# Kernel optimization log

Measured on AMD Instinct MI355X. Metric: run time of the kernel, lower is better.

Reference implementation:

```python
import math
import jax, jax.numpy as jnp
import numpy as np

B, N, D, H, PREFIX = 2, 2048, 2048, 16, 512
HD = D // H
ROPE_BASE = 10000.0

def _rope(x):
    # x: [b, h, n, d]; rotate-half RoPE with positions 0..n-1
    d = x.shape[-1]
    n = x.shape[-2]
    inv_freq = 1.0 / (ROPE_BASE ** (jnp.arange(0, d, 2, dtype=jnp.float32) / d))  # [d/2]
    pos = jnp.arange(n, dtype=jnp.float32)
    freqs = pos[:, None] * inv_freq[None, :]            # [n, d/2]
    cos, sin = jnp.cos(freqs), jnp.sin(freqs)
    x1, x2 = x[..., : d // 2], x[..., d // 2 :]
    return jnp.concatenate([x1 * cos - x2 * sin, x2 * cos + x1 * sin], axis=-1).astype(x.dtype)

def setup_inputs() -> dict:
    key = jax.random.key(0)
    ks = jax.random.split(key, 6)
    x = jax.random.normal(ks[0], (B, N, D), dtype=jnp.float32)
    prefix_k = jax.random.normal(ks[1], (B, H, PREFIX, HD), dtype=jnp.float32)
    prefix_v = jax.random.normal(ks[2], (B, H, PREFIX, HD), dtype=jnp.float32)
    Wqkv = jax.random.normal(ks[3], (D, 3 * D), dtype=jnp.float32) * (D ** -0.5)
    bqkv = jnp.zeros((3 * D,), dtype=jnp.float32)
    Wff = jax.random.normal(ks[4], (D, D), dtype=jnp.float32) * (D ** -0.5)
    bff = jnp.zeros((D,), dtype=jnp.float32)
    # causal mask over current tokens; prefix (cache) columns fully visible
    causal = jnp.tril(jnp.ones((N, N), dtype=jnp.int32))
    mask = jnp.concatenate([jnp.ones((N, PREFIX), dtype=jnp.int32), causal], axis=1)[None, None]  # [1,1,N,N+PREFIX]
    return {"x": x, "mask": mask, "prefix_k": prefix_k, "prefix_v": prefix_v,
            "Wqkv": Wqkv, "bqkv": bqkv, "Wff": Wff, "bff": bff}

def reference(x, mask, prefix_k, prefix_v, Wqkv, bqkv, Wff, bff):
    b, n, d = x.shape
    h = prefix_k.shape[1]
    hd = d // h
    qkv = (x @ Wqkv + bqkv).reshape(b, n, 3, h, hd)      # 'b n (c h d)'
    qkv = jnp.transpose(qkv, (2, 0, 3, 1, 4))            # -> c b h n d
    q, k, v = qkv[0], qkv[1], qkv[2]
    k = jnp.concatenate([prefix_k, k], axis=2)           # [b,h,kt,hd]
    v = jnp.concatenate([prefix_v, v], axis=2)
    next_prefix_kv = jnp.stack([k, v])                   # cached BEFORE rope (as in source)
    q = _rope(q)
    k = _rope(k)
    scores = jnp.einsum('bhqd,bhkd->bhqk', q, k) / math.sqrt(hd)
    scores = jnp.where(mask == 0, jnp.finfo(scores.dtype).min, scores)
    probs = jax.nn.softmax(scores, axis=-1)              # dropout_prob=0.0 -> identity
    attn_o = jnp.einsum('bhqk,bhkd->bhqd', probs, v)
    attn_o = jnp.transpose(attn_o, (0, 2, 1, 3)).reshape(b, n, d)
    return attn_o @ Wff + bff, next_prefix_kv
```

## Files before the change

kernel.cpp:

```cpp
#include <hip/hip_runtime.h>
#include <hip/hip_bf16.h>
#include <stdint.h>

#define TPB 256

using f32x4 = __attribute__((ext_vector_type(4))) float;
using s16x8 = __attribute__((ext_vector_type(8))) short;
using s16x4 = __attribute__((ext_vector_type(4))) short;

__device__ __forceinline__ short f2bf(float f){
  union { float f; uint32_t u; } v; v.f = f;
  uint32_t u = v.u;
  uint32_t r = (u + 0x7fffu + ((u >> 16) & 1u)) >> 16;
  return (short)(uint16_t)r;
}
__device__ __forceinline__ float bf2f(short b){
  union { uint32_t u; float f; } v; v.u = ((uint32_t)(uint16_t)b) << 16;
  return v.f;
}
__device__ __forceinline__ f32x4 mfma16(s16x8 a, s16x8 b, f32x4 c){
  return __builtin_amdgcn_mfma_f32_16x16x32_bf16(a, b, c, 0, 0, 0);
}

#define AS1(p) ((const __attribute__((address_space(1))) void*)(p))
#define AS3(p) ((__attribute__((address_space(3))) void*)(p))

__global__ void k_cvt_bf16(const float* __restrict__ src, short* __restrict__ dst, int n8){
  int i = blockIdx.x * TPB + threadIdx.x;
  if (i >= n8) return;
  const float4* s4 = (const float4*)src;
  float4 a = s4[2*i], b = s4[2*i+1];
  s16x8 o;
  o[0]=f2bf(a.x); o[1]=f2bf(a.y); o[2]=f2bf(a.z); o[3]=f2bf(a.w);
  o[4]=f2bf(b.x); o[5]=f2bf(b.y); o[6]=f2bf(b.z); o[7]=f2bf(b.w);
  *(s16x8*)(dst + 8*(size_t)i) = o;
}

__global__ void k_trans_cvt(const float* __restrict__ W, short* __restrict__ WT, int K, int Nn){
  __shared__ float ls[32][33];
  int k0 = blockIdx.x * 32, n0 = blockIdx.y * 32;
  int c = threadIdx.x & 31, i = threadIdx.x >> 5;
#pragma unroll
  for (int rr = 0; rr < 4; rr++){
    int row = i*4 + rr;
    ls[row][c] = W[(size_t)(k0+row)*Nn + n0 + c];
  }
  __syncthreads();
#pragma unroll
  for (int rr = 0; rr < 4; rr++){
    int ro = i*4 + rr;
    WT[(size_t)(n0+ro)*K + k0 + c] = f2bf(ls[c][ro]);
  }
}

template<int EPI>
__global__ void __launch_bounds__(512, 2) k_gemm8(
    const short* __restrict__ A, const short* __restrict__ Bt,
    int Nn, int K,
    const float* __restrict__ bias,
    float* __restrict__ outp,
    float* __restrict__ kvout,
    short* __restrict__ qpre, short* __restrict__ kpre, short* __restrict__ vpre)
{
  __shared__ __align__(16) short As[3][16384];
  __shared__ __align__(16) short Bs[3][8192];
  const int tid = threadIdx.x;
  const int w = tid >> 6, l = tid & 63;
  const int lrow = l & 15, lg = l >> 4;
  const int wm = w >> 1, wn = w & 1;
  const int m0 = blockIdx.x << 8, n0 = blockIdx.y << 7;
  const int NT = K >> 6;

  f32x4 acc[4][4] = {};

#define STAGE_A(slot, t, j) do {                                             \
    int chunk = ((w*4 + (j)) << 6) + l;                                      \
    int row = chunk >> 3, cc = chunk & 7;                                    \
    __builtin_amdgcn_global_load_lds(                                        \
      AS1(A + (size_t)(m0+row)*K + (t)*64 + ((cc ^ (row&7)) << 3)),          \
      AS3(&As[slot][(w*4 + (j)) << 9]), 16, 0, 0);                           \
  } while(0)
#define STAGE_B(slot, t, j) do {                                             \
    int chunk = ((w*2 + (j)) << 6) + l;                                      \
    int row = chunk >> 3, cc = chunk & 7;                                    \
    __builtin_amdgcn_global_load_lds(                                        \
      AS1(Bt + (size_t)(n0+row)*K + (t)*64 + ((cc ^ (row&7)) << 3)),         \
      AS3(&Bs[slot][(w*2 + (j)) << 9]), 16, 0, 0);                           \
  } while(0)

  STAGE_A(0,0,0); STAGE_A(0,0,1); STAGE_A(0,0,2); STAGE_A(0,0,3);
  STAGE_B(0,0,0); STAGE_B(0,0,1);
  STAGE_A(1,1,0); STAGE_A(1,1,1); STAGE_A(1,1,2); STAGE_A(1,1,3);
  STAGE_B(1,1,0); STAGE_B(1,1,1);

  int slot = 0;
  for (int t = 0; t < NT; ++t){
    if (t < NT-1) asm volatile("s_waitcnt vmcnt(6)" ::: "memory");
    else          asm volatile("s_waitcnt vmcnt(0)" ::: "memory");
    __builtin_amdgcn_s_barrier();
    asm volatile("" ::: "memory");
    const int sslot = (slot == 0) ? 2 : slot - 1;
    const bool st = (t+2) < NT;
    const char* ab = (const char*)As[slot];
    const char* bb = (const char*)Bs[slot];

    s16x8 bfr[4][2];
#pragma unroll
    for (int ni = 0; ni < 4; ni++){
      int row = wn*64 + ni*16 + lrow;
#pragma unroll
      for (int ks = 0; ks < 2; ks++)
        bfr[ni][ks] = *(const s16x8*)(bb + row*128 + ((ks*64 + lg*16) ^ ((row&7)<<4)));
    }
    s16x8 af[2][2];
#pragma unroll
    for (int mi = 0; mi < 2; mi++){
      int row = wm*64 + mi*16 + lrow;
#pragma unroll
      for (int ks = 0; ks < 2; ks++)
        af[mi][ks] = *(const s16x8*)(ab + row*128 + ((ks*64 + lg*16) ^ ((row&7)<<4)));
    }
    if (st){ STAGE_A(sslot,t+2,0); STAGE_A(sslot,t+2,1); STAGE_B(sslot,t+2,0); }
    __builtin_amdgcn_s_setprio(1);
#pragma unroll
    for (int ks = 0; ks < 2; ks++)
#pragma unroll
      for (int mi = 0; mi < 2; mi++)
#pragma unroll
        for (int ni = 0; ni < 4; ni++)
          acc[mi][ni] = mfma16(af[mi][ks], bfr[ni][ks], acc[mi][ni]);
    __builtin_amdgcn_s_setprio(0);
    asm volatile("" ::: "memory");
    __builtin_amdgcn_s_barrier();
    asm volatile("" ::: "memory");

    s16x8 af2[2][2];
#pragma unroll
    for (int mi = 0; mi < 2; mi++){
      int row = wm*64 + (mi+2)*16 + lrow;
#pragma unroll
      for (int ks = 0; ks < 2; ks++)
        af2[mi][ks] = *(const s16x8*)(ab + row*128 + ((ks*64 + lg*16) ^ ((row&7)<<4)));
    }
    if (st){ STAGE_A(sslot,t+2,2); STAGE_A(sslot,t+2,3); STAGE_B(sslot,t+2,1); }
    __builtin_amdgcn_s_setprio(1);
#pragma unroll
    for (int ks = 0; ks < 2; ks++)
#pragma unroll
      for (int mi = 0; mi < 2; mi++)
#pragma unroll
        for (int ni = 0; ni < 4; ni++)
          acc[mi+2][ni] = mfma16(af2[mi][ks], bfr[ni][ks], acc[mi+2][ni]);
    __builtin_amdgcn_s_setprio(0);
    slot = (slot == 2) ? 0 : slot + 1;
  }
#undef STAGE_A
#undef STAGE_B

#pragma unroll
  for (int mi = 0; mi < 4; mi++){
#pragma unroll
    for (int ni = 0; ni < 4; ni++){
      const int c  = n0 + wn*64 + ni*16 + lrow;
      const int mb = m0 + wm*64 + mi*16 + lg*4;
      const float bv = bias[c];
      if (EPI == 1){
#pragma unroll
        for (int r = 0; r < 4; r++)
          outp[(size_t)(mb+r)*Nn + c] = acc[mi][ni][r] + bv;
      } else {
        const int s = c >> 11, h = (c >> 7) & 15, tt = c & 127;
#pragma unroll
        for (int r = 0; r < 4; r++){
          const int m = mb + r;
          const int b = m >> 11, n = m & 2047;
          const int bh = b*16 + h;
          const float val = acc[mi][ni][r] + bv;
          if (s == 0){
            qpre[((size_t)bh*2048 + n)*128 + tt] = f2bf(val);
          } else if (s == 1){
            kvout[((size_t)bh*2560 + 512 + n)*128 + tt] = val;
            kpre[((size_t)bh*2048 + n)*128 + tt] = f2bf(val);
          } else {
            kvout[(size_t)(32 + bh)*327680 + (size_t)(512 + n)*128 + tt] = val;
            vpre[((size_t)bh*2048 + n)*128 + tt] = f2bf(val);
          }
        }
      }
    }
  }
}

__global__ void k_rope_k_new(const short* __restrict__ kpre, short* __restrict__ kr){
  int gid = blockIdx.x * TPB + threadIdx.x;
  int jb = (gid & 7) * 8; size_t row = gid >> 3;
  int bh = (int)(row >> 11), n = (int)(row & 2047);
  int pos = 512 + n;
  s16x8 v1 = *(const s16x8*)&kpre[row*128 + jb];
  s16x8 v2 = *(const s16x8*)&kpre[row*128 + 64 + jb];
  s16x8 o1, o2;
#pragma unroll
  for (int e = 0; e < 8; e++){
    float invf = __expf((float)(jb + e) * (-9.210340371976184f/64.0f));
    float sn, cs; __sincosf((float)pos * invf, &sn, &cs);
    float x1 = bf2f(v1[e]), x2 = bf2f(v2[e]);
    o1[e] = f2bf(x1*cs - x2*sn);
    o2[e] = f2bf(x2*cs + x1*sn);
  }
  size_t drow = (size_t)bh*2560 + pos;
  *(s16x8*)&kr[drow*128 + jb]      = o1;
  *(s16x8*)&kr[drow*128 + 64 + jb] = o2;
}

__global__ void k_rope_k_prefix(const float* __restrict__ pk, float* __restrict__ kvout0,
                                short* __restrict__ kr){
  int gid = blockIdx.x * TPB + threadIdx.x;
  int jb = (gid & 7) * 8; size_t row = gid >> 3;
  int bh = (int)(row >> 9), p = (int)(row & 511);
  float4 a1 = *(const float4*)&pk[row*128 + jb];
  float4 a2 = *(const float4*)&pk[row*128 + jb + 4];
  float4 b1 = *(const float4*)&pk[row*128 + 64 + jb];
  float4 b2 = *(const float4*)&pk[row*128 + 64 + jb + 4];
  size_t orow = (size_t)bh*2560 + p;
  *(float4*)&kvout0[orow*128 + jb]          = a1;
  *(float4*)&kvout0[orow*128 + jb + 4]      = a2;
  *(float4*)&kvout0[orow*128 + 64 + jb]     = b1;
  *(float4*)&kvout0[orow*128 + 64 + jb + 4] = b2;
  float x1[8] = {a1.x,a1.y,a1.z,a1.w,a2.x,a2.y,a2.z,a2.w};
  float x2[8] = {b1.x,b1.y,b1.z,b1.w,b2.x,b2.y,b2.z,b2.w};
  s16x8 o1, o2;
#pragma unroll
  for (int e = 0; e < 8; e++){
    float invf = __expf((float)(jb + e) * (-9.210340371976184f/64.0f));
    float sn, cs; __sincosf((float)p * invf, &sn, &cs);
    o1[e] = f2bf(x1[e]*cs - x2[e]*sn);
    o2[e] = f2bf(x2[e]*cs + x1[e]*sn);
  }
  *(s16x8*)&kr[orow*128 + jb]      = o1;
  *(s16x8*)&kr[orow*128 + 64 + jb] = o2;
}

__global__ void k_v_prefix(const float* __restrict__ pv, float* __restrict__ kvout1,
                           short* __restrict__ vT){
  __shared__ float ls[32][129];
  int bh = blockIdx.x >> 4, pt = blockIdx.x & 15;
  int p0 = pt*32, tid = threadIdx.x;
#pragma unroll
  for (int i = 0; i < 16; i++){
    int idx = i*TPB + tid; int p = idx >> 7, t = idx & 127;
    float v = pv[((size_t)bh*512 + p0 + p)*128 + t];
    ls[p][t] = v;
    kvout1[((size_t)bh*2560 + p0 + p)*128 + t] = v;
  }
  __syncthreads();
#pragma unroll
  for (int i = 0; i < 16; i++){
    int idx = i*TPB + tid; int t = idx >> 5, p = idx & 31;
    vT[((size_t)bh*128 + t)*2560 + p0 + p] = f2bf(ls[p][t]);
  }
}

__global__ void k_v_new(const short* __restrict__ vpre, short* __restrict__ vT){
  __shared__ float ls[32][129];
  int bh = blockIdx.x >> 6, nt = blockIdx.x & 63;
  int n0 = nt*32, tid = threadIdx.x;
#pragma unroll
  for (int i = 0; i < 16; i++){
    int idx = i*TPB + tid; int p = idx >> 7, t = idx & 127;
    ls[p][t] = bf2f(vpre[((size_t)bh*2048 + n0 + p)*128 + t]);
  }
  __syncthreads();
#pragma unroll
  for (int i = 0; i < 16; i++){
    int idx = i*TPB + tid; int t = idx >> 5, p = idx & 31;
    vT[((size_t)bh*128 + t)*2560 + 512 + n0 + p] = f2bf(ls[p][t]);
  }
}

__global__ void __launch_bounds__(256, 2) k_attn(
    const short* __restrict__ qr, const short* __restrict__ kr,
    const short* __restrict__ vT, short* __restrict__ attno)
{
  __shared__ short Ks[2][64*128];
  __shared__ short VTs[2][128*64];
  __shared__ short Ps[4][16*64];
  const int bh = blockIdx.x;
  const int pA = blockIdx.y, pB = 31 - pA;
  const int nA = 9 + pA, nTot = 49;
  const int tid = threadIdx.x, w = tid >> 6, l = tid & 63;
  const int lrow = l & 15, lg = l >> 4;
  const int b = bh >> 4, h = bh & 15;

  s16x8 qfA[4], qfB[4];
  {
    const int nAr = pA*64 + w*16 + lrow;
    const int nBr = pB*64 + w*16 + lrow;
    const size_t rA = (size_t)bh*2048 + nAr;
    const size_t rB = (size_t)bh*2048 + nBr;
#pragma unroll
    for (int ks = 0; ks < 4; ks++){
      qfA[ks] = *(const s16x8*)&qr[rA*128 + ks*32 + lg*8];
      qfB[ks] = *(const s16x8*)&qr[rB*128 + ks*32 + lg*8];
    }
    const float sc = 0.088388347648318447f;
#pragma unroll
    for (int ks = 0; ks < 2; ks++){
#pragma unroll
      for (int e = 0; e < 8; e++){
        const int j = ks*32 + lg*8 + e;
        const float invf = __expf((float)j * (-9.210340371976184f/64.0f));
        float sn, cs;
        __sincosf((float)nAr * invf, &sn, &cs);
        float x1 = bf2f(qfA[ks][e]), x2 = bf2f(qfA[ks+2][e]);
        qfA[ks][e]   = f2bf((x1*cs - x2*sn) * sc);
        qfA[ks+2][e] = f2bf((x2*cs + x1*sn) * sc);
        __sincosf((float)nBr * invf, &sn, &cs);
        float y1 = bf2f(qfB[ks][e]), y2 = bf2f(qfB[ks+2][e]);
        qfB[ks][e]   = f2bf((y1*cs - y2*sn) * sc);
        qfB[ks+2][e] = f2bf((y2*cs + y1*sn) * sc);
      }
    }
  }

#define STAGE_KV(buf, kv0s) do {                                                    \
    _Pragma("unroll")                                                               \
    for (int i_ = 0; i_ < 4; i_++){                                                 \
      int chunk = i_*256 + tid;                                                     \
      int row = chunk >> 4, cc = (chunk & 15) ^ (row & 7);                          \
      __builtin_amdgcn_global_load_lds(                                             \
        AS1(kr + ((size_t)bh*2560 + (kv0s) + row)*128 + cc*8),                      \
        AS3((char*)Ks[buf] + (i_*256 + w*64)*16), 16, 0, 0);                        \
    }                                                                               \
    _Pragma("unroll")                                                               \
    for (int i_ = 0; i_ < 4; i_++){                                                 \
      int chunk = i_*256 + tid;                                                     \
      int row = chunk >> 3, cc = (chunk & 7) ^ (row & 7);                           \
      __builtin_amdgcn_global_load_lds(                                             \
        AS1(vT + ((size_t)bh*128 + row)*2560 + (kv0s) + cc*8),                      \
        AS3((char*)VTs[buf] + (i_*256 + w*64)*16), 16, 0, 0);                       \
    }                                                                               \
  } while(0)

  STAGE_KV(0, 0);
  STAGE_KV(1, 64);

  char* psw = (char*)&Ps[w][0];
  int g = 0;
#pragma unroll 2
  for (int ph = 0; ph < 2; ph++){
    const int qt = ph ? pB : pA;
    const int n = 9 + qt;
    const int qbw = qt*64 + w*16;
    f32x4 acc[8] = {};
    float mr = -1e30f, lsum = 0.f;

    for (int t = 0; t < n; t++, g++){
      if (g+1 < nTot) asm volatile("s_waitcnt vmcnt(8)" ::: "memory");
      else            asm volatile("s_waitcnt vmcnt(0)" ::: "memory");
      __builtin_amdgcn_s_barrier();
      asm volatile("" ::: "memory");
      const char* kb_ = (const char*)Ks[g&1];
      const char* vb_ = (const char*)VTs[g&1];
      const int kv0 = t*64;

      f32x4 sf[4];
      __builtin_amdgcn_s_setprio(1);
#pragma unroll
      for (int kb = 0; kb < 4; kb++){
        f32x4 s = {0.f,0.f,0.f,0.f};
#pragma unroll
        for (int ks = 0; ks < 4; ks++){
          int row  = kb*16 + lrow;
          int colb = ks*64 + lg*16;
          s16x8 kf = *(const s16x8*)(kb_ + row*256 + (colb ^ ((row&7)<<4)));
          s = mfma16(kf, ph ? qfB[ks] : qfA[ks], s);
        }
        sf[kb] = s;
      }
      __builtin_amdgcn_s_setprio(0);

      const int qme = 512 + qbw + lrow;
      if (kv0 + 63 > 512 + qbw){
#pragma unroll
        for (int kb = 0; kb < 4; kb++)
#pragma unroll
          for (int r = 0; r < 4; r++){
            int kg = kv0 + kb*16 + lg*4 + r;
            if (kg > qme) sf[kb][r] = -1e30f;
          }
      }

      float m_ = fmaxf(
          fmaxf(fmaxf(fmaxf(sf[0][0],sf[0][1]),fmaxf(sf[0][2],sf[0][3])),
                fmaxf(fmaxf(sf[1][0],sf[1][1]),fmaxf(sf[1][2],sf[1][3]))),
          fmaxf(fmaxf(fmaxf(sf[2][0],sf[2][1]),fmaxf(sf[2][2],sf[2][3])),
                fmaxf(fmaxf(sf[3][0],sf[3][1]),fmaxf(sf[3][2],sf[3][3]))));
      m_ = fmaxf(m_, __shfl_xor(m_, 16));
      m_ = fmaxf(m_, __shfl_xor(m_, 32));

      if (__any(m_ > mr + 8.f)){
        float mnew = fmaxf(mr, m_);
        float sc = __expf(mr - mnew);
        mr = mnew;
        lsum *= sc;
        float scr[4];
#pragma unroll
        for (int r = 0; r < 4; r++)
          scr[r] = __shfl(sc, (l & 48) | (lg*4 + r));
#pragma unroll
        for (int dt = 0; dt < 8; dt++)
#pragma unroll
          for (int r = 0; r < 4; r++) acc[dt][r] *= scr[r];
      }

#pragma unroll
      for (int kb = 0; kb < 4; kb++){
        float p0 = __expf(sf[kb][0] - mr);
        float p1 = __expf(sf[kb][1] - mr);
        float p2 = __expf(sf[kb][2] - mr);
        float p3 = __expf(sf[kb][3] - mr);
        lsum += (p0+p1)+(p2+p3);
        s16x4 pk4 = { f2bf(p0), f2bf(p1), f2bf(p2), f2bf(p3) };
        *(s16x4*)(psw + (lrow*128 + ((kb*32 + lg*8) ^ ((lrow&7)<<4)))) = pk4;
      }

      __builtin_amdgcn_s_setprio(1);
#pragma unroll
      for (int kp = 0; kp < 2; kp++){
        s16x8 pa = *(const s16x8*)(psw + (lrow*128 + ((kp*64 + lg*16) ^ ((lrow&7)<<4))));
#pragma unroll
        for (int dt = 0; dt < 8; dt++){
          int vrow = dt*16 + lrow;
          int vcolb = kp*64 + lg*16;
          s16x8 vf = *(const s16x8*)(vb_ + vrow*128 + (vcolb ^ ((vrow&7)<<4)));
          acc[dt] = mfma16(pa, vf, acc[dt]);
        }
      }
      __builtin_amdgcn_s_setprio(0);

      asm volatile("" ::: "memory");
      __builtin_amdgcn_s_barrier();
      asm volatile("" ::: "memory");
      const int gg = g + 2;
      if (gg < nTot){
        const int kvs = (gg < nA ? gg : gg - nA) * 64;
        STAGE_KV(g&1, kvs);
      }
    }

    float ls_ = lsum;
    ls_ += __shfl_xor(ls_, 16);
    ls_ += __shfl_xor(ls_, 32);
    float linv[4];
#pragma unroll
    for (int r = 0; r < 4; r++)
      linv[r] = 1.f / __shfl(ls_, (l & 48) | (lg*4 + r));
#pragma unroll
    for (int dt = 0; dt < 8; dt++){
#pragma unroll
      for (int r = 0; r < 4; r++){
        int nrow = qbw + lg*4 + r;
        int dcol = h*128 + dt*16 + lrow;
        attno[((size_t)b*2048 + nrow)*2048 + dcol] = f2bf(acc[dt][r] * linv[r]);
      }
    }
  }
#undef STAGE_KV
}

extern "C" void kernel_launch(void* const* d_in, const int* in_sizes, int n_in,
                              void* d_out, int out_size, void* d_ws, size_t ws_size,
                              hipStream_t stream)
{
  const float* x    = (const float*)d_in[0];
  const float* pk   = (const float*)d_in[2];
  const float* pv   = (const float*)d_in[3];
  const float* Wqkv = (const float*)d_in[4];
  const float* bqkv = (const float*)d_in[5];
  const float* Wff  = (const float*)d_in[6];
  const float* bff  = (const float*)d_in[7];
  float* out   = (float*)d_out;
  float* kvout = out + 8388608;

  char* ws = (char*)d_ws;
  short* xb    = (short*)(ws);
  short* wqkvT = (short*)(ws + 16777216);
  short* wffT  = (short*)(ws + 41943040);
  short* qpre  = (short*)(ws + 50331648);
  short* kpre  = (short*)(ws + 67108864);
  short* vpre  = (short*)(ws + 83886080);
  short* krp   = (short*)(ws + 117440512);
  short* vTp   = (short*)(ws + 138412032);
  short* attno = (short*)(ws + 159383552);

  k_cvt_bf16<<<4096, TPB, 0, stream>>>(x, xb, 1048576);
  k_trans_cvt<<<dim3(64, 192), TPB, 0, stream>>>(Wqkv, wqkvT, 2048, 6144);
  k_trans_cvt<<<dim3(64, 64),  TPB, 0, stream>>>(Wff,  wffT,  2048, 2048);

  k_gemm8<0><<<dim3(16, 48), 512, 0, stream>>>(xb, wqkvT, 6144, 2048, bqkv,
                                               nullptr, kvout, qpre, kpre, vpre);

  k_rope_k_new<<<2048, TPB, 0, stream>>>(kpre, krp);
  k_rope_k_prefix<<<512, TPB, 0, stream>>>(pk, kvout, krp);
  k_v_prefix<<<512, TPB, 0, stream>>>(pv, kvout + (size_t)32*327680, vTp);
  k_v_new<<<2048, TPB, 0, stream>>>(vpre, vTp);

  k_attn<<<dim3(32, 16), TPB, 0, stream>>>(qpre, krp, vTp, attno);

  k_gemm8<1><<<dim3(16, 16), 512, 0, stream>>>(attno, wffT, 2048, 2048, bff,
                                               out, nullptr, nullptr, nullptr, nullptr);
}
```

Before: 307.1 us.

## Double query rows per attention wave to reuse K/V tiles across two 16-row blocks

Each wave now processes 32 query rows (two 16-row MFMA blocks) instead of 16, so every K and V fragment loaded from LDS feeds two MFMAs. The query tile per block grows to 128 rows, the grid is halved to 256 blocks, and launch bounds drop to one block per SIMD set. This cuts LDS and global K/V traffic per query, at the cost of doubled accumulator registers, lower occupancy, and fewer blocks to spread across the GPU's compute units.

```diff
diff --git a/kernel.cpp b/kernel.cpp
--- a/kernel.cpp
+++ b/kernel.cpp
@@ -277,47 +277,50 @@
   }
 }
 
-__global__ void __launch_bounds__(256, 2) k_attn(
+__global__ void __launch_bounds__(256, 1) k_attn(
     const short* __restrict__ qr, const short* __restrict__ kr,
     const short* __restrict__ vT, short* __restrict__ attno)
 {
   __shared__ short Ks[2][64*128];
   __shared__ short VTs[2][128*64];
-  __shared__ short Ps[4][16*64];
+  __shared__ short Ps[4][32*64 + 64];
   const int bh = blockIdx.x;
-  const int pA = blockIdx.y, pB = 31 - pA;
-  const int nA = 9 + pA, nTot = 49;
+  const int pA = blockIdx.y, pB = 15 - pA;
+  const int nA = 10 + 2*pA, nTot = 50;
   const int tid = threadIdx.x, w = tid >> 6, l = tid & 63;
   const int lrow = l & 15, lg = l >> 4;
   const int b = bh >> 4, h = bh & 15;
 
-  s16x8 qfA[4], qfB[4];
+  s16x8 qfA[2][4], qfB[2][4];
   {
-    const int nAr = pA*64 + w*16 + lrow;
-    const int nBr = pB*64 + w*16 + lrow;
-    const size_t rA = (size_t)bh*2048 + nAr;
-    const size_t rB = (size_t)bh*2048 + nBr;
-#pragma unroll
-    for (int ks = 0; ks < 4; ks++){
-      qfA[ks] = *(const s16x8*)&qr[rA*128 + ks*32 + lg*8];
-      qfB[ks] = *(const s16x8*)&qr[rB*128 + ks*32 + lg*8];
-    }
     const float sc = 0.088388347648318447f;
 #pragma unroll
-    for (int ks = 0; ks < 2; ks++){
-#pragma unroll
-      for (int e = 0; e < 8; e++){
-        const int j = ks*32 + lg*8 + e;
-        const float invf = __expf((float)j * (-9.210340371976184f/64.0f));
-        float sn, cs;
-        __sincosf((float)nAr * invf, &sn, &cs);
-        float x1 = bf2f(qfA[ks][e]), x2 = bf2f(qfA[ks+2][e]);
-        qfA[ks][e]   = f2bf((x1*cs - x2*sn) * sc);
-        qfA[ks+2][e] = f2bf((x2*cs + x1*sn) * sc);
-        __sincosf((float)nBr * invf, &sn, &cs);
-        float y1 = bf2f(qfB[ks][e]), y2 = bf2f(qfB[ks+2][e]);
-        qfB[ks][e]   = f2bf((y1*cs - y2*sn) * sc);
-        qfB[ks+2][e] = f2bf((y2*cs + y1*sn) * sc);
+    for (int qb = 0; qb < 2; qb++){
+      const int nAr = pA*128 + w*32 + qb*16 + lrow;
+      const int nBr = pB*128 + w*32 + qb*16 + lrow;
+      const size_t rA = (size_t)bh*2048 + nAr;
+      const size_t rB = (size_t)bh*2048 + nBr;
+#pragma unroll
+      for (int ks = 0; ks < 4; ks++){
+        qfA[qb][ks] = *(const s16x8*)&qr[rA*128 + ks*32 + lg*8];
+        qfB[qb][ks] = *(const s16x8*)&qr[rB*128 + ks*32 + lg*8];
+      }
+#pragma unroll
+      for (int ks = 0; ks < 2; ks++){
+#pragma unroll
+        for (int e = 0; e < 8; e++){
+          const int j = ks*32 + lg*8 + e;
+          const float invf = __expf((float)j * (-9.210340371976184f/64.0f));
+          float sn, cs;
+          __sincosf((float)nAr * invf, &sn, &cs);
+          float x1 = bf2f(qfA[qb][ks][e]), x2 = bf2f(qfA[qb][ks+2][e]);
+          qfA[qb][ks][e]   = f2bf((x1*cs - x2*sn) * sc);
+          qfA[qb][ks+2][e] = f2bf((x2*cs + x1*sn) * sc);
+          __sincosf((float)nBr * invf, &sn, &cs);
+          float y1 = bf2f(qfB[qb][ks][e]), y2 = bf2f(qfB[qb][ks+2][e]);
+          qfB[qb][ks][e]   = f2bf((y1*cs - y2*sn) * sc);
+          qfB[qb][ks+2][e] = f2bf((y2*cs + y1*sn) * sc);
+        }
       }
     }
   }
@@ -349,10 +352,11 @@
 #pragma unroll 2
   for (int ph = 0; ph < 2; ph++){
     const int qt = ph ? pB : pA;
-    const int n = 9 + qt;
-    const int qbw = qt*64 + w*16;
-    f32x4 acc[8] = {};
-    float mr = -1e30f, lsum = 0.f;
+    const int n = 10 + 2*qt;
+    const int qbw = qt*128 + w*32;
+    f32x4 acc0[8] = {}, acc1[8] = {};
+    float mr0 = -1e30f, ls0 = 0.f;
+    float mr1 = -1e30f, ls1 = 0.f;
 
     for (int t = 0; t < n; t++, g++){
       if (g+1 < nTot) asm volatile("s_waitcnt vmcnt(8)" ::: "memory");
@@ -363,77 +367,113 @@
       const char* vb_ = (const char*)VTs[g&1];
       const int kv0 = t*64;
 
-      f32x4 sf[4];
+      f32x4 sf0[4], sf1[4];
       __builtin_amdgcn_s_setprio(1);
 #pragma unroll
       for (int kb = 0; kb < 4; kb++){
-        f32x4 s = {0.f,0.f,0.f,0.f};
+        f32x4 s0 = {0.f,0.f,0.f,0.f}, s1 = {0.f,0.f,0.f,0.f};
 #pragma unroll
         for (int ks = 0; ks < 4; ks++){
           int row  = kb*16 + lrow;
           int colb = ks*64 + lg*16;
           s16x8 kf = *(const s16x8*)(kb_ + row*256 + (colb ^ ((row&7)<<4)));
-          s = mfma16(kf, ph ? qfB[ks] : qfA[ks], s);
-        }
-        sf[kb] = s;
+          s0 = mfma16(kf, ph ? qfB[0][ks] : qfA[0][ks], s0);
+          s1 = mfma16(kf, ph ? qfB[1][ks] : qfA[1][ks], s1);
+        }
+        sf0[kb] = s0; sf1[kb] = s1;
       }
       __builtin_amdgcn_s_setprio(0);
 
-      const int qme = 512 + qbw + lrow;
       if (kv0 + 63 > 512 + qbw){
+        const int qme0 = 512 + qbw + lrow;
+        const int qme1 = qme0 + 16;
 #pragma unroll
         for (int kb = 0; kb < 4; kb++)
 #pragma unroll
           for (int r = 0; r < 4; r++){
             int kg = kv0 + kb*16 + lg*4 + r;
-            if (kg > qme) sf[kb][r] = -1e30f;
+            if (kg > qme0) sf0[kb][r] = -1e30f;
+            if (kg > qme1) sf1[kb][r] = -1e30f;
           }
       }
 
-      float m_ = fmaxf(
-          fmaxf(fmaxf(fmaxf(sf[0][0],sf[0][1]),fmaxf(sf[0][2],sf[0][3])),
-                fmaxf(fmaxf(sf[1][0],sf[1][1]),fmaxf(sf[1][2],sf[1][3]))),
-          fmaxf(fmaxf(fmaxf(sf[2][0],sf[2][1]),fmaxf(sf[2][2],sf[2][3])),
-                fmaxf(fmaxf(sf[3][0],sf[3][1]),fmaxf(sf[3][2],sf[3][3]))));
-      m_ = fmaxf(m_, __shfl_xor(m_, 16));
-      m_ = fmaxf(m_, __shfl_xor(m_, 32));
-
-      if (__any(m_ > mr + 8.f)){
-        float mnew = fmaxf(mr, m_);
-        float sc = __expf(mr - mnew);
-        mr = mnew;
-        lsum *= sc;
-        float scr[4];
-#pragma unroll
-        for (int r = 0; r < 4; r++)
-          scr[r] = __shfl(sc, (l & 48) | (lg*4 + r));
-#pragma unroll
-        for (int dt = 0; dt < 8; dt++)
-#pragma unroll
-          for (int r = 0; r < 4; r++) acc[dt][r] *= scr[r];
-      }
-
-#pragma unroll
-      for (int kb = 0; kb < 4; kb++){
-        float p0 = __expf(sf[kb][0] - mr);
-        float p1 = __expf(sf[kb][1] - mr);
-        float p2 = __expf(sf[kb][2] - mr);
-        float p3 = __expf(sf[kb][3] - mr);
-        lsum += (p0+p1)+(p2+p3);
-        s16x4 pk4 = { f2bf(p0), f2bf(p1), f2bf(p2), f2bf(p3) };
-        *(s16x4*)(psw + (lrow*128 + ((kb*32 + lg*8) ^ ((lrow&7)<<4)))) = pk4;
+      {
+        float m_ = fmaxf(
+            fmaxf(fmaxf(fmaxf(sf0[0][0],sf0[0][1]),fmaxf(sf0[0][2],sf0[0][3])),
+                  fmaxf(fmaxf(sf0[1][0],sf0[1][1]),fmaxf(sf0[1][2],sf0[1][3]))),
+            fmaxf(fmaxf(fmaxf(sf0[2][0],sf0[2][1]),fmaxf(sf0[2][2],sf0[2][3])),
+                  fmaxf(fmaxf(sf0[3][0],sf0[3][1]),fmaxf(sf0[3][2],sf0[3][3]))));
+        m_ = fmaxf(m_, __shfl_xor(m_, 16));
+        m_ = fmaxf(m_, __shfl_xor(m_, 32));
+        if (__any(m_ > mr0 + 8.f)){
+          float mnew = fmaxf(mr0, m_);
+          float sc = __expf(mr0 - mnew);
+          mr0 = mnew; ls0 *= sc;
+          float scr[4];
+#pragma unroll
+          for (int r = 0; r < 4; r++)
+            scr[r] = __shfl(sc, (l & 48) | (lg*4 + r));
+#pragma unroll
+          for (int dt = 0; dt < 8; dt++)
+#pragma unroll
+            for (int r = 0; r < 4; r++) acc0[dt][r] *= scr[r];
+        }
+#pragma unroll
+        for (int kb = 0; kb < 4; kb++){
+          float p0 = __expf(sf0[kb][0] - mr0);
+          float p1 = __expf(sf0[kb][1] - mr0);
+          float p2 = __expf(sf0[kb][2] - mr0);
+          float p3 = __expf(sf0[kb][3] - mr0);
+          ls0 += (p0+p1)+(p2+p3);
+          s16x4 pk4 = { f2bf(p0), f2bf(p1), f2bf(p2), f2bf(p3) };
+          *(s16x4*)(psw + (lrow*128 + ((kb*32 + lg*8) ^ ((lrow&7)<<4)))) = pk4;
+        }
+      }
+      {
+        float m_ = fmaxf(
+            fmaxf(fmaxf(fmaxf(sf1[0][0],sf1[0][1]),fmaxf(sf1[0][2],sf1[0][3])),
+                  fmaxf(fmaxf(sf1[1][0],sf1[1][1]),fmaxf(sf1[1][2],sf1[1][3]))),
+            fmaxf(fmaxf(fmaxf(sf1[2][0],sf1[2][1]),fmaxf(sf1[2][2],sf1[2][3])),
+                  fmaxf(fmaxf(sf1[3][0],sf1[3][1]),fmaxf(sf1[3][2],sf1[3][3]))));
+        m_ = fmaxf(m_, __shfl_xor(m_, 16));
+        m_ = fmaxf(m_, __shfl_xor(m_, 32));
+        if (__any(m_ > mr1 + 8.f)){
+          float mnew = fmaxf(mr1, m_);
+          float sc = __expf(mr1 - mnew);
+          mr1 = mnew; ls1 *= sc;
+          float scr[4];
+#pragma unroll
+          for (int r = 0; r < 4; r++)
+            scr[r] = __shfl(sc, (l & 48) | (lg*4 + r));
+#pragma unroll
+          for (int dt = 0; dt < 8; dt++)
+#pragma unroll
+            for (int r = 0; r < 4; r++) acc1[dt][r] *= scr[r];
+        }
+#pragma unroll
+        for (int kb = 0; kb < 4; kb++){
+          float p0 = __expf(sf1[kb][0] - mr1);
+          float p1 = __expf(sf1[kb][1] - mr1);
+          float p2 = __expf(sf1[kb][2] - mr1);
+          float p3 = __expf(sf1[kb][3] - mr1);
+          ls1 += (p0+p1)+(p2+p3);
+          s16x4 pk4 = { f2bf(p0), f2bf(p1), f2bf(p2), f2bf(p3) };
+          *(s16x4*)(psw + ((16 + lrow)*128 + ((kb*32 + lg*8) ^ ((lrow&7)<<4)))) = pk4;
+        }
       }
 
       __builtin_amdgcn_s_setprio(1);
 #pragma unroll
       for (int kp = 0; kp < 2; kp++){
-        s16x8 pa = *(const s16x8*)(psw + (lrow*128 + ((kp*64 + lg*16) ^ ((lrow&7)<<4))));
+        s16x8 pa0 = *(const s16x8*)(psw + (lrow*128       + ((kp*64 + lg*16) ^ ((lrow&7)<<4))));
+        s16x8 pa1 = *(const s16x8*)(psw + ((16+lrow)*128  + ((kp*64 + lg*16) ^ ((lrow&7)<<4))));
 #pragma unroll
         for (int dt = 0; dt < 8; dt++){
           int vrow = dt*16 + lrow;
           int vcolb = kp*64 + lg*16;
           s16x8 vf = *(const s16x8*)(vb_ + vrow*128 + (vcolb ^ ((vrow&7)<<4)));
-          acc[dt] = mfma16(pa, vf, acc[dt]);
+          acc0[dt] = mfma16(pa0, vf, acc0[dt]);
+          acc1[dt] = mfma16(pa1, vf, acc1[dt]);
         }
       }
       __builtin_amdgcn_s_setprio(0);
@@ -448,20 +488,27 @@
       }
     }
 
-    float ls_ = lsum;
-    ls_ += __shfl_xor(ls_, 16);
-    ls_ += __shfl_xor(ls_, 32);
-    float linv[4];
-#pragma unroll
-    for (int r = 0; r < 4; r++)
-      linv[r] = 1.f / __shfl(ls_, (l & 48) | (lg*4 + r));
+    float lsa = ls0;
+    lsa += __shfl_xor(lsa, 16);
+    lsa += __shfl_xor(lsa, 32);
+    float lsb = ls1;
+    lsb += __shfl_xor(lsb, 16);
+    lsb += __shfl_xor(lsb, 32);
+    float linv0[4], linv1[4];
+#pragma unroll
+    for (int r = 0; r < 4; r++){
+      linv0[r] = 1.f / __shfl(lsa, (l & 48) | (lg*4 + r));
+      linv1[r] = 1.f / __shfl(lsb, (l & 48) | (lg*4 + r));
+    }
 #pragma unroll
     for (int dt = 0; dt < 8; dt++){
 #pragma unroll
       for (int r = 0; r < 4; r++){
-        int nrow = qbw + lg*4 + r;
-        int dcol = h*128 + dt*16 + lrow;
-        attno[((size_t)b*2048 + nrow)*2048 + dcol] = f2bf(acc[dt][r] * linv[r]);
+        const int dcol = h*128 + dt*16 + lrow;
+        const int nrow0 = qbw + lg*4 + r;
+        const int nrow1 = qbw + 16 + lg*4 + r;
+        attno[((size_t)b*2048 + nrow0)*2048 + dcol] = f2bf(acc0[dt][r] * linv0[r]);
+        attno[((size_t)b*2048 + nrow1)*2048 + dcol] = f2bf(acc1[dt][r] * linv1[r]);
       }
     }
   }
@@ -505,7 +552,7 @@
   k_v_prefix<<<512, TPB, 0, stream>>>(pv, kvout + (size_t)32*327680, vTp);
   k_v_new<<<2048, TPB, 0, stream>>>(vpre, vTp);
 
-  k_attn<<<dim3(32, 16), TPB, 0, stream>>>(qpre, krp, vTp, attno);
+  k_attn<<<dim3(32, 8), 256, 0, stream>>>(qpre, krp, vTp, attno);
 
   k_gemm8<1><<<dim3(16, 16), 512, 0, stream>>>(attno, wffT, 2048, 2048, bff,
                                                out, nullptr, nullptr, nullptr, nullptr);
```

After: 329.9 us. 1.07x slower.
